# Kernel optimization log

Measured on AMD Instinct MI355X. Metric: run time of the kernel, lower is better.

## Reference

```python
import jax, jax.numpy as jnp
import numpy as np

B, D, S, E = 32768, 512, 128, 8


def setup_inputs() -> dict:
    key = jax.random.key(0)
    ks = jax.random.split(key, 8)
    x = jax.random.normal(ks[0], (B, D), dtype=jnp.float32)
    y_index = jax.random.randint(ks[1], (B, 1), 0, E, dtype=jnp.int32)
    y_hard = jax.random.uniform(ks[2], (B, E), dtype=jnp.float32)
    z = jax.random.normal(ks[3], (B, 1), dtype=jnp.float32)
    # per-branch 2-layer MLP params, kaiming-ish scaling
    W1 = jax.random.normal(ks[4], (E, D, S), dtype=jnp.float32) / np.sqrt(D)
    b1 = jax.random.normal(ks[5], (E, S), dtype=jnp.float32) * 0.01
    W2 = jax.random.normal(ks[6], (E, S, D), dtype=jnp.float32) / np.sqrt(S)
    b2 = jax.random.normal(ks[7], (E, D), dtype=jnp.float32) * 0.01
    return {"x": x, "y_index": y_index, "y_hard": y_hard, "z": z,
            "W1": W1, "b1": b1, "W2": W2, "b2": b2}


def reference(x, y_index, y_hard, z, W1, b1, W2, b2):
    # out = relu(x); each token b routed to branch y_index[b];
    # branch MLP: relu(out @ W1[e] + b1[e]) @ W2[e] + b2[e], scaled by z, plus residual.
    # y_hard unused (eval path / backward_on_y_hard=False).
    n_branches = W1.shape[0]
    yi = y_index[:, 0]                                   # [B]
    onehot = jax.nn.one_hot(yi, n_branches, dtype=x.dtype)  # [B,E]
    out = jax.nn.relu(x)                                 # [B,D]
    h = jax.nn.relu(jnp.einsum('bd,eds->bes', out, W1) + b1[None])  # [B,E,S]
    h_sel = jnp.einsum('bes,be->bs', h, onehot)          # [B,S] hidden of routed branch
    o = jnp.einsum('bs,esd->bed', h_sel, W2)             # [B,E,D]
    o_sel = jnp.einsum('bed,be->bd', o, onehot) + b2[yi] # [B,D]
    return x + o_sel * z
```

## Files before the change

### kernel.cpp

```cpp
#include <hip/hip_runtime.h>
#include <hip/hip_bf16.h>

#define NB 32768
#define ND 512
#define NS 128
#define NE 8
#define TPE 96

typedef __attribute__((ext_vector_type(8))) short bf16x8;
typedef __attribute__((ext_vector_type(4))) float f32x4;

__device__ __forceinline__ unsigned short f2b(float f) {
  union { __hip_bfloat16 h; unsigned short u; } cv;
  cv.h = __float2bfloat16(f);
  return cv.u;
}

__device__ __forceinline__ bf16x8 relu_cvt8v(float4 a, float4 b) {
  bf16x8 r;
  r[0] = (short)f2b(fmaxf(a.x, 0.f)); r[1] = (short)f2b(fmaxf(a.y, 0.f));
  r[2] = (short)f2b(fmaxf(a.z, 0.f)); r[3] = (short)f2b(fmaxf(a.w, 0.f));
  r[4] = (short)f2b(fmaxf(b.x, 0.f)); r[5] = (short)f2b(fmaxf(b.y, 0.f));
  r[6] = (short)f2b(fmaxf(b.z, 0.f)); r[7] = (short)f2b(fmaxf(b.w, 0.f));
  return r;
}

__device__ __forceinline__ void gload16(const void* gsrc, void* ldst) {
  __builtin_amdgcn_global_load_lds(
      (const __attribute__((address_space(1))) unsigned int*)gsrc,
      (__attribute__((address_space(3))) unsigned int*)ldst, 16, 0, 0);
}

#define BARV6  asm volatile("s_waitcnt vmcnt(6)\n\ts_barrier" ::: "memory")
#define BARV12 asm volatile("s_waitcnt vmcnt(12)\n\ts_barrier" ::: "memory")
#define BARV10 asm volatile("s_waitcnt vmcnt(10)\n\ts_barrier" ::: "memory")
#define BARV0  asm volatile("s_waitcnt vmcnt(0)\n\ts_barrier" ::: "memory")
#define BARV2L asm volatile("s_waitcnt vmcnt(2) lgkmcnt(0)\n\ts_barrier" ::: "memory")
#define CFENCE asm volatile("" ::: "memory")

__global__ void zero_counts_k(int* counts) {
  if (threadIdx.x < NE) counts[threadIdx.x] = 0;
}

__global__ void bin_rows_k(const int* __restrict__ yidx, int* __restrict__ counts,
                           int* __restrict__ bucket) {
  __shared__ int lcnt[NE];
  __shared__ int lbase[NE];
  int tid = threadIdx.x;
  if (tid < NE) lcnt[tid] = 0;
  __syncthreads();
  int b = blockIdx.x * blockDim.x + tid;
  int e = yidx[b];
  int pos = atomicAdd(&lcnt[e], 1);
  __syncthreads();
  if (tid < NE) lbase[tid] = atomicAdd(&counts[tid], lcnt[tid]);
  __syncthreads();
  bucket[e * NB + lbase[e] + pos] = b;
}

__global__ void transpose_cvt_k(const float* __restrict__ in,
                                unsigned short* __restrict__ out, int R, int C) {
  __shared__ float lt[32][33];
  int tpm = (R >> 5) * (C >> 5);
  int mat = blockIdx.x / tpm;
  int rem = blockIdx.x % tpm;
  int tcn = C >> 5;
  int tr = rem / tcn, tc = rem % tcn;
  const float* mi = in + (size_t)mat * R * C;
  unsigned short* mo = out + (size_t)mat * R * C;
  int r = threadIdx.x >> 5, c = threadIdx.x & 31;
#pragma unroll
  for (int i = 0; i < 4; ++i) {
    int rr = r + i * 8;
    lt[rr][c] = mi[(size_t)(tr * 32 + rr) * C + tc * 32 + c];
  }
  __syncthreads();
#pragma unroll
  for (int i = 0; i < 4; ++i) {
    int rr = r + i * 8;
    int orow = tc * 32 + rr;
    int d = tr * 32 + c;
    int ocol = (d & ~63) | ((d & 63) ^ ((orow & 7) << 3));
    mo[(size_t)orow * R + ocol] = f2b(lt[c][rr]);
  }
}

#define M1LOADX(DST, c)                                 \
  do {                                                  \
    const float* xp = xrow + (c) * 64;                  \
    DST[0] = *(const float4*)(xp);                      \
    DST[1] = *(const float4*)(xp + 4);                  \
    DST[2] = *(const float4*)(xp + 32);                 \
    DST[3] = *(const float4*)(xp + 36);                 \
  } while (0)

#define M1STAGE(c)                                                        \
  do {                                                                    \
    gload16(g0 + (c) * 128, (char*)wt[(c) % 3] + p0 * 16);                \
    gload16(g1 + (c) * 128, (char*)wt[(c) % 3] + p1 * 16);                \
  } while (0)

#define M1_ITER(c, CUR)                                                        \
  do {                                                                         \
    if ((c) <= 5) { M1STAGE((c) + 2); }                                        \
    bf16x8 a0 = relu_cvt8v(CUR[0], CUR[1]);                                    \
    bf16x8 a1 = relu_cvt8v(CUR[2], CUR[3]);                                    \
    if ((c) <= 5) { M1LOADX(CUR, (c) + 2); }                                   \
    const unsigned short* wb = wt[(c) % 3];                                    \
    _Pragma("unroll") for (int nt = 0; nt < 4; ++nt) {                         \
      int n = nh * 64 + nt * 16 + l15;                                         \
      int sw = (n & 7) << 3;                                                   \
      bf16x8 b0 = *(const bf16x8*)&wb[n * 64 + ((l4 * 8) ^ sw)];               \
      bf16x8 b1v = *(const bf16x8*)&wb[n * 64 + ((32 + l4 * 8) ^ sw)];         \
      acc[nt] = __builtin_amdgcn_mfma_f32_16x16x32_bf16(a0, b0, acc[nt], 0, 0, 0);  \
      acc[nt] = __builtin_amdgcn_mfma_f32_16x16x32_bf16(a1, b1v, acc[nt], 0, 0, 0); \
    }                                                                          \
    if ((c) <= 5) { BARV6; } else if ((c) == 6) { BARV0; }                     \
  } while (0)

#define M2STAGE(c)                                                           \
  do {                                                                       \
    gload16(w2e + (c) * 16384 + p0 * 16, (char*)wt[(c) % 3] + p0 * 16);      \
    gload16(w2e + (c) * 16384 + p1 * 16, (char*)wt[(c) % 3] + p1 * 16);      \
  } while (0)

#define M2_ITER(c)                                                            \
  do {                                                                        \
    if ((c) <= 5) { M2STAGE((c) + 2); }                                       \
    float xe0[4], xe1[4];                                                     \
    int d0 = (c) * 64 + nh * 32 + l15;                                        \
    int d1 = d0 + 16;                                                         \
    _Pragma("unroll") for (int r = 0; r < 4; ++r) {                           \
      xe0[r] = x[(size_t)orow[r] * ND + d0];                                  \
      xe1[r] = x[(size_t)orow[r] * ND + d1];                                  \
    }                                                                         \
    float bias0 = b2[e * ND + d0];                                            \
    float bias1 = b2[e * ND + d1];                                            \
    const unsigned short* wb = wt[(c) % 3];                                   \
    f32x4 acc0 = (f32x4){0.f, 0.f, 0.f, 0.f};                                 \
    f32x4 acc1 = (f32x4){0.f, 0.f, 0.f, 0.f};                                 \
    _Pragma("unroll") for (int kk = 0; kk < 4; ++kk) {                        \
      int dl0 = nh * 32 + l15;                                                \
      int sw0 = (dl0 & 7) << 3;                                               \
      bf16x8 bv0 = *(const bf16x8*)&wb[dl0 * 128 + ((kk * 32 + l4 * 8) ^ sw0)]; \
      acc0 = __builtin_amdgcn_mfma_f32_16x16x32_bf16(ha[kk], bv0, acc0, 0, 0, 0); \
      int dl1 = nh * 32 + 16 + l15;                                           \
      int sw1 = (dl1 & 7) << 3;                                               \
      bf16x8 bv1 = *(const bf16x8*)&wb[dl1 * 128 + ((kk * 32 + l4 * 8) ^ sw1)]; \
      acc1 = __builtin_amdgcn_mfma_f32_16x16x32_bf16(ha[kk], bv1, acc1, 0, 0, 0); \
    }                                                                         \
    _Pragma("unroll") for (int r = 0; r < 4; ++r) {                           \
      float r0 = xe0[r] + (acc0[r] + bias0) * zr[r];                          \
      float r1 = xe1[r] + (acc1[r] + bias1) * zr[r];                          \
      float* p0s = valid[r] ? (out + (size_t)orow[r] * ND + d0) : (osink + tid); \
      float* p1s = valid[r] ? (out + (size_t)orow[r] * ND + d1) : (osink + tid); \
      *p0s = r0;                                                              \
      *p1s = r1;                                                              \
    }                                                                         \
    if ((c) <= 5) { BARV12; } else if ((c) == 6) { BARV10; }                  \
  } while (0)

__launch_bounds__(512, 2)
__global__ void moe_f(const float* __restrict__ x, const float* __restrict__ z,
                      const float* __restrict__ b1, const float* __restrict__ b2,
                      const unsigned short* __restrict__ w1sw,
                      const unsigned short* __restrict__ w2sw,
                      const int* __restrict__ counts, const int* __restrict__ bucket,
                      float* __restrict__ out, float* __restrict__ osink) {
  __shared__ unsigned short wt[3][8192];
  __shared__ unsigned short ht[64][136];
  int e = blockIdx.x & 7;
  int t = blockIdx.x >> 3;
  int cnt = counts[e];
  if (t * 64 >= cnt) return;
  int tid = threadIdx.x, w = tid >> 6, lane = tid & 63;
  int l15 = lane & 15, l4 = lane >> 4;
  int rg = w >> 1, nh = w & 1;

  int ra = t * 64 + rg * 16 + l15;
  int ras = (ra < cnt) ? ra : (cnt - 1);
  int rid = bucket[e * NB + ras];
  const float* xrow = x + (size_t)rid * ND + l4 * 8;

  const char* w1e = (const char*)w1sw + (size_t)e * NS * ND * 2;
  const char* w2e = (const char*)w2sw + (size_t)e * ND * NS * 2;
  int p0 = tid, p1 = tid + 512;
  const char* g0 = w1e + (p0 >> 3) * 1024 + (p0 & 7) * 16;
  const char* g1 = w1e + (p1 >> 3) * 1024 + (p1 & 7) * 16;

  float4 xA[4], xB[4];
  M1LOADX(xA, 0);
  M1STAGE(0);
  CFENCE;
  M1LOADX(xB, 1);
  M1STAGE(1);
  BARV6;

  f32x4 acc[4];
#pragma unroll
  for (int i = 0; i < 4; ++i) acc[i] = (f32x4){0.f, 0.f, 0.f, 0.f};

  M1_ITER(0, xA); M1_ITER(1, xB); M1_ITER(2, xA); M1_ITER(3, xB);
  M1_ITER(4, xA); M1_ITER(5, xB); M1_ITER(6, xA); M1_ITER(7, xB);

#pragma unroll
  for (int nt = 0; nt < 4; ++nt) {
    int col = nh * 64 + nt * 16 + l15;
    float bias = b1[e * NS + col];
#pragma unroll
    for (int r = 0; r < 4; ++r)
      ht[rg * 16 + l4 * 4 + r][col] = f2b(fmaxf(acc[nt][r] + bias, 0.f));
  }

  int orow[4];
  bool valid[4];
  float zr[4];
#pragma unroll
  for (int r = 0; r < 4; ++r) {
    int pos = t * 64 + rg * 16 + l4 * 4 + r;
    valid[r] = (pos < cnt);
    int ps = valid[r] ? pos : (cnt - 1);
    orow[r] = bucket[e * NB + ps];
    zr[r] = z[orow[r]];
  }

  M2STAGE(0);
  CFENCE;
  M2STAGE(1);
  BARV2L;

  bf16x8 ha[4];
#pragma unroll
  for (int kk = 0; kk < 4; ++kk)
    ha[kk] = *(const bf16x8*)&ht[rg * 16 + l15][kk * 32 + l4 * 8];

  M2_ITER(0); M2_ITER(1); M2_ITER(2); M2_ITER(3);
  M2_ITER(4); M2_ITER(5); M2_ITER(6); M2_ITER(7);
}

extern "C" void kernel_launch(void* const* d_in, const int* in_sizes, int n_in,
                              void* d_out, int out_size, void* d_ws, size_t ws_size,
                              hipStream_t stream) {
  const float* x = (const float*)d_in[0];
  const int* yidx = (const int*)d_in[1];
  const float* z = (const float*)d_in[3];
  const float* W1 = (const float*)d_in[4];
  const float* b1 = (const float*)d_in[5];
  const float* W2 = (const float*)d_in[6];
  const float* b2 = (const float*)d_in[7];
  float* out = (float*)d_out;

  char* ws = (char*)d_ws;
  int* counts = (int*)ws;
  int* bucket = (int*)(ws + 256);
  size_t off = 256 + (size_t)NE * NB * 4;
  unsigned short* w1sw = (unsigned short*)(ws + off);
  off += (size_t)NE * NS * ND * 2;
  unsigned short* w2sw = (unsigned short*)(ws + off);
  off += (size_t)NE * ND * NS * 2;
  float* osink = (float*)(ws + off);

  zero_counts_k<<<1, 64, 0, stream>>>(counts);
  bin_rows_k<<<NB / 1024, 1024, 0, stream>>>(yidx, counts, bucket);
  transpose_cvt_k<<<NE * (ND / 32) * (NS / 32), 256, 0, stream>>>(W1, w1sw, ND, NS);
  transpose_cvt_k<<<NE * (NS / 32) * (ND / 32), 256, 0, stream>>>(W2, w2sw, NS, ND);
  moe_f<<<NE * TPE, 512, 0, stream>>>(x, z, b1, b2, w1sw, w2sw, counts, bucket,
                                      out, osink);
}
```

Before: 67.28 us.

## Stage activations and outputs through LDS for coalesced global access

Each block now loads its 64 gathered x rows once, applies ReLU, converts them to bf16 and writes them into a swizzled LDS tile that the first GEMM reads, replacing per-iteration register loads of x. The second GEMM writes its accumulators into an LDS output buffer that aliases the x tile. Two write phases then apply the b2 bias, the z scaling and the residual using full-row float4 loads and stores, replacing scattered 4-byte stores and the sink buffer. LDS use grows to roughly 133KB, so launch bounds drop to one block per CU, trading occupancy for coalescing and fewer redundant global reads.

```diff
diff --git a/kernel.cpp b/kernel.cpp
--- a/kernel.cpp
+++ b/kernel.cpp
@@ -31,10 +31,10 @@
       (__attribute__((address_space(3))) unsigned int*)ldst, 16, 0, 0);
 }
 
-#define BARV6  asm volatile("s_waitcnt vmcnt(6)\n\ts_barrier" ::: "memory")
-#define BARV12 asm volatile("s_waitcnt vmcnt(12)\n\ts_barrier" ::: "memory")
-#define BARV10 asm volatile("s_waitcnt vmcnt(10)\n\ts_barrier" ::: "memory")
+#define BARV2  asm volatile("s_waitcnt vmcnt(2)\n\ts_barrier" ::: "memory")
 #define BARV0  asm volatile("s_waitcnt vmcnt(0)\n\ts_barrier" ::: "memory")
+#define BARL   asm volatile("s_waitcnt lgkmcnt(0)\n\ts_barrier" ::: "memory")
+#define BARV17 asm volatile("s_waitcnt vmcnt(17)\n\ts_barrier" ::: "memory")
 #define BARV2L asm volatile("s_waitcnt vmcnt(2) lgkmcnt(0)\n\ts_barrier" ::: "memory")
 #define CFENCE asm volatile("" ::: "memory")
 
@@ -85,27 +85,19 @@
   }
 }
 
-#define M1LOADX(DST, c)                                 \
-  do {                                                  \
-    const float* xp = xrow + (c) * 64;                  \
-    DST[0] = *(const float4*)(xp);                      \
-    DST[1] = *(const float4*)(xp + 4);                  \
-    DST[2] = *(const float4*)(xp + 32);                 \
-    DST[3] = *(const float4*)(xp + 36);                 \
-  } while (0)
-
 #define M1STAGE(c)                                                        \
   do {                                                                    \
     gload16(g0 + (c) * 128, (char*)wt[(c) % 3] + p0 * 16);                \
     gload16(g1 + (c) * 128, (char*)wt[(c) % 3] + p1 * 16);                \
   } while (0)
 
-#define M1_ITER(c, CUR)                                                        \
+#define S1_ITER(c)                                                             \
   do {                                                                         \
     if ((c) <= 5) { M1STAGE((c) + 2); }                                        \
-    bf16x8 a0 = relu_cvt8v(CUR[0], CUR[1]);                                    \
-    bf16x8 a1 = relu_cvt8v(CUR[2], CUR[3]);                                    \
-    if ((c) <= 5) { M1LOADX(CUR, (c) + 2); }                                   \
+    bf16x8 a0 = *(const bf16x8*)((const char*)&xt[arow][0] +                   \
+                 ((((c) * 64 + l4 * 8) * 2) ^ arsw));                          \
+    bf16x8 a1 = *(const bf16x8*)((const char*)&xt[arow][0] +                   \
+                 ((((c) * 64 + 32 + l4 * 8) * 2) ^ arsw));                     \
     const unsigned short* wb = wt[(c) % 3];                                    \
     _Pragma("unroll") for (int nt = 0; nt < 4; ++nt) {                         \
       int n = nh * 64 + nt * 16 + l15;                                         \
@@ -115,7 +107,7 @@
       acc[nt] = __builtin_amdgcn_mfma_f32_16x16x32_bf16(a0, b0, acc[nt], 0, 0, 0);  \
       acc[nt] = __builtin_amdgcn_mfma_f32_16x16x32_bf16(a1, b1v, acc[nt], 0, 0, 0); \
     }                                                                          \
-    if ((c) <= 5) { BARV6; } else if ((c) == 6) { BARV0; }                     \
+    if ((c) <= 5) { BARV2; } else if ((c) == 6) { BARV0; }                     \
   } while (0)
 
 #define M2STAGE(c)                                                           \
@@ -124,18 +116,9 @@
     gload16(w2e + (c) * 16384 + p1 * 16, (char*)wt[(c) % 3] + p1 * 16);      \
   } while (0)
 
-#define M2_ITER(c)                                                            \
+#define S2_ITER(c)                                                            \
   do {                                                                        \
     if ((c) <= 5) { M2STAGE((c) + 2); }                                       \
-    float xe0[4], xe1[4];                                                     \
-    int d0 = (c) * 64 + nh * 32 + l15;                                        \
-    int d1 = d0 + 16;                                                         \
-    _Pragma("unroll") for (int r = 0; r < 4; ++r) {                           \
-      xe0[r] = x[(size_t)orow[r] * ND + d0];                                  \
-      xe1[r] = x[(size_t)orow[r] * ND + d1];                                  \
-    }                                                                         \
-    float bias0 = b2[e * ND + d0];                                            \
-    float bias1 = b2[e * ND + d1];                                            \
     const unsigned short* wb = wt[(c) % 3];                                   \
     f32x4 acc0 = (f32x4){0.f, 0.f, 0.f, 0.f};                                 \
     f32x4 acc1 = (f32x4){0.f, 0.f, 0.f, 0.f};                                 \
@@ -149,26 +132,46 @@
       bf16x8 bv1 = *(const bf16x8*)&wb[dl1 * 128 + ((kk * 32 + l4 * 8) ^ sw1)]; \
       acc1 = __builtin_amdgcn_mfma_f32_16x16x32_bf16(ha[kk], bv1, acc1, 0, 0, 0); \
     }                                                                         \
+    int cc = (c) & 3;                                                         \
     _Pragma("unroll") for (int r = 0; r < 4; ++r) {                           \
-      float r0 = xe0[r] + (acc0[r] + bias0) * zr[r];                          \
-      float r1 = xe1[r] + (acc1[r] + bias1) * zr[r];                          \
-      float* p0s = valid[r] ? (out + (size_t)orow[r] * ND + d0) : (osink + tid); \
-      float* p1s = valid[r] ? (out + (size_t)orow[r] * ND + d1) : (osink + tid); \
-      *p0s = r0;                                                              \
-      *p1s = r1;                                                              \
+      obuf[rg * 16 + l4 * 4 + r][cc * 64 + nh * 32 + l15] = acc0[r];          \
+      obuf[rg * 16 + l4 * 4 + r][cc * 64 + nh * 32 + 16 + l15] = acc1[r];     \
     }                                                                         \
-    if ((c) <= 5) { BARV12; } else if ((c) == 6) { BARV10; }                  \
-  } while (0)
-
-__launch_bounds__(512, 2)
+  } while (0)
+
+#define WRITE_PHASE(h)                                                        \
+  do {                                                                        \
+    float4 b24 = *(const float4*)&b2[e * ND + (h) * 256 + lane * 4];          \
+    _Pragma("unroll") for (int j = 0; j < 8; ++j) {                           \
+      int row = w * 8 + j;                                                    \
+      float4 o4 = *(const float4*)&obuf[row][lane * 4];                       \
+      int rid = rowid_s[row];                                                 \
+      float zv = zs[row];                                                     \
+      float4 x4 = *(const float4*)&x[(size_t)rid * ND + (h) * 256 + lane * 4];\
+      float4 res;                                                             \
+      res.x = x4.x + (o4.x + b24.x) * zv;                                     \
+      res.y = x4.y + (o4.y + b24.y) * zv;                                     \
+      res.z = x4.z + (o4.z + b24.z) * zv;                                     \
+      res.w = x4.w + (o4.w + b24.w) * zv;                                     \
+      *(float4*)&out[(size_t)rid * ND + (h) * 256 + lane * 4] = res;          \
+    }                                                                         \
+  } while (0)
+
+__launch_bounds__(512, 1)
 __global__ void moe_f(const float* __restrict__ x, const float* __restrict__ z,
                       const float* __restrict__ b1, const float* __restrict__ b2,
                       const unsigned short* __restrict__ w1sw,
                       const unsigned short* __restrict__ w2sw,
                       const int* __restrict__ counts, const int* __restrict__ bucket,
-                      float* __restrict__ out, float* __restrict__ osink) {
+                      float* __restrict__ out) {
+  __shared__ __align__(16) char xo_raw[64 * 520 * 2];
   __shared__ unsigned short wt[3][8192];
   __shared__ unsigned short ht[64][136];
+  __shared__ int rowid_s[64];
+  __shared__ float zs[64];
+  auto xt = (unsigned short(*)[520])xo_raw;
+  auto obuf = (float(*)[260])xo_raw;
+
   int e = blockIdx.x & 7;
   int t = blockIdx.x >> 3;
   int cnt = counts[e];
@@ -177,10 +180,26 @@
   int l15 = lane & 15, l4 = lane >> 4;
   int rg = w >> 1, nh = w & 1;
 
-  int ra = t * 64 + rg * 16 + l15;
-  int ras = (ra < cnt) ? ra : (cnt - 1);
-  int rid = bucket[e * NB + ras];
-  const float* xrow = x + (size_t)rid * ND + l4 * 8;
+  if (tid < 64) {
+    int pos = t * 64 + tid;
+    int ps = (pos < cnt) ? pos : (cnt - 1);
+    int rid = bucket[e * NB + ps];
+    rowid_s[tid] = rid;
+    zs[tid] = z[rid];
+  }
+
+#pragma unroll
+  for (int j = 0; j < 8; ++j) {
+    int row = w * 8 + j;
+    int pos = t * 64 + row;
+    int ps = (pos < cnt) ? pos : (cnt - 1);
+    int rid = bucket[e * NB + ps];
+    const float* xp = x + (size_t)rid * ND + lane * 8;
+    float4 a = *(const float4*)xp;
+    float4 b = *(const float4*)(xp + 4);
+    bf16x8 v = relu_cvt8v(a, b);
+    *(bf16x8*)((char*)&xt[row][0] + ((lane * 16) ^ ((row & 7) << 4))) = v;
+  }
 
   const char* w1e = (const char*)w1sw + (size_t)e * NS * ND * 2;
   const char* w2e = (const char*)w2sw + (size_t)e * ND * NS * 2;
@@ -188,20 +207,21 @@
   const char* g0 = w1e + (p0 >> 3) * 1024 + (p0 & 7) * 16;
   const char* g1 = w1e + (p1 >> 3) * 1024 + (p1 & 7) * 16;
 
-  float4 xA[4], xB[4];
-  M1LOADX(xA, 0);
+  __syncthreads();
+
   M1STAGE(0);
   CFENCE;
-  M1LOADX(xB, 1);
   M1STAGE(1);
-  BARV6;
+  BARV2;
 
   f32x4 acc[4];
 #pragma unroll
   for (int i = 0; i < 4; ++i) acc[i] = (f32x4){0.f, 0.f, 0.f, 0.f};
-
-  M1_ITER(0, xA); M1_ITER(1, xB); M1_ITER(2, xA); M1_ITER(3, xB);
-  M1_ITER(4, xA); M1_ITER(5, xB); M1_ITER(6, xA); M1_ITER(7, xB);
+  int arow = rg * 16 + l15;
+  int arsw = (arow & 7) << 4;
+
+  S1_ITER(0); S1_ITER(1); S1_ITER(2); S1_ITER(3);
+  S1_ITER(4); S1_ITER(5); S1_ITER(6); S1_ITER(7);
 
 #pragma unroll
   for (int nt = 0; nt < 4; ++nt) {
@@ -211,19 +231,6 @@
     for (int r = 0; r < 4; ++r)
       ht[rg * 16 + l4 * 4 + r][col] = f2b(fmaxf(acc[nt][r] + bias, 0.f));
   }
-
-  int orow[4];
-  bool valid[4];
-  float zr[4];
-#pragma unroll
-  for (int r = 0; r < 4; ++r) {
-    int pos = t * 64 + rg * 16 + l4 * 4 + r;
-    valid[r] = (pos < cnt);
-    int ps = valid[r] ? pos : (cnt - 1);
-    orow[r] = bucket[e * NB + ps];
-    zr[r] = z[orow[r]];
-  }
-
   M2STAGE(0);
   CFENCE;
   M2STAGE(1);
@@ -234,8 +241,17 @@
   for (int kk = 0; kk < 4; ++kk)
     ha[kk] = *(const bf16x8*)&ht[rg * 16 + l15][kk * 32 + l4 * 8];
 
-  M2_ITER(0); M2_ITER(1); M2_ITER(2); M2_ITER(3);
-  M2_ITER(4); M2_ITER(5); M2_ITER(6); M2_ITER(7);
+  S2_ITER(0); BARV2;
+  S2_ITER(1); BARV2;
+  S2_ITER(2); BARV2;
+  S2_ITER(3); BARL;
+  WRITE_PHASE(0);
+  BARV17;
+  S2_ITER(4); BARV2;
+  S2_ITER(5); BARV2;
+  S2_ITER(6); BARV0;
+  S2_ITER(7); BARL;
+  WRITE_PHASE(1);
 }
 
 extern "C" void kernel_launch(void* const* d_in, const int* in_sizes, int n_in,
@@ -257,13 +273,10 @@
   unsigned short* w1sw = (unsigned short*)(ws + off);
   off += (size_t)NE * NS * ND * 2;
   unsigned short* w2sw = (unsigned short*)(ws + off);
-  off += (size_t)NE * ND * NS * 2;
-  float* osink = (float*)(ws + off);
 
   zero_counts_k<<<1, 64, 0, stream>>>(counts);
   bin_rows_k<<<NB / 1024, 1024, 0, stream>>>(yidx, counts, bucket);
   transpose_cvt_k<<<NE * (ND / 32) * (NS / 32), 256, 0, stream>>>(W1, w1sw, ND, NS);
   transpose_cvt_k<<<NE * (NS / 32) * (ND / 32), 256, 0, stream>>>(W2, w2sw, NS, ND);
-  moe_f<<<NE * TPE, 512, 0, stream>>>(x, z, b1, b2, w1sw, w2sw, counts, bucket,
-                                      out, osink);
-}
+  moe_f<<<NE * TPE, 512, 0, stream>>>(x, z, b1, b2, w1sw, w2sw, counts, bucket, out);
+}
```

New measurement: 71.48 us. 1.06x slower.
